# Kernel optimization log

Hardware: AMD Instinct MI355X
Metric: run time of the kernel (lower is better)

The kernel has to match this reference:

```python
import jax, jax.numpy as jnp
import numpy as np

B, T, IN, OUT, R = 4096, 8, 1024, 1024, 32

def setup_inputs() -> dict:
    key = jax.random.key(0)
    k1, k2, k3, k4 = jax.random.split(key, 4)
    return {
        "x": jax.random.normal(k1, (B, T, IN), dtype=jnp.float32),
        "first_shared_core": jax.random.normal(k2, (T, R), dtype=jnp.float32) * 0.1,
        "middle_shared_core": jax.random.normal(k3, (R, IN, R), dtype=jnp.float32) * 0.1,
        "task_core": jax.random.normal(k4, (R, OUT), dtype=jnp.float32) * 0.1,
    }

def reference(x, first_shared_core, middle_shared_core, task_core):
    # contract TT cores -> per-task weight [T, IN, OUT]
    w = jnp.einsum('tj,jik->tik', first_shared_core, middle_shared_core)
    w = jnp.einsum('tik,ko->tio', w, task_core)
    # per-task batched matmul: [B,T,IN] x [T,IN,OUT] -> [B,T,OUT]
    return jnp.einsum('bti,tio->bto', x, w)
```

## Files before the change

### kernel.cpp

```cpp
#include <hip/hip_runtime.h>
#include <hip/hip_bf16.h>
#include <stdint.h>

#define B_DIM 4096
#define T_DIM 8
#define IN_DIM 1024
#define OUT_DIM 1024
#define R_DIM 32

#define BM 256
#define BN 256
#define BK 64
#define NKT (IN_DIM / BK)

typedef __bf16 bf16x8 __attribute__((ext_vector_type(8)));
typedef float  f32x4  __attribute__((ext_vector_type(4)));

#define VMCNT(n) asm volatile("s_waitcnt vmcnt(" #n ")" ::: "memory")
#define CFENCE() asm volatile("" ::: "memory")
#define BARRIER() do { CFENCE(); __builtin_amdgcn_s_barrier(); CFENCE(); } while (0)


__device__ __forceinline__ uint32_t pack2_bf16(float a, float b) {
  uint32_t ua = __float_as_uint(a), ub = __float_as_uint(b);
  ua = (ua + 0x7FFFu + ((ua >> 16) & 1u)) >> 16;
  ub = (ub + 0x7FFFu + ((ub >> 16) & 1u)) & 0xFFFF0000u;
  return ua | ub;
}

__device__ __forceinline__ void gload_lds16(const void* g, void* l) {
  __builtin_amdgcn_global_load_lds(
      (const __attribute__((address_space(1))) void*)(uintptr_t)g,
      (__attribute__((address_space(3))) void*)(uint32_t)(uintptr_t)l,
      16, 0, 0);
}

__device__ __forceinline__ void stage_half(const uint16_t* gtile, int ktn,
                                           int half, uint8_t* ldsop,
                                           int wave, int lane) {
#pragma unroll
  for (int j = 0; j < 2; ++j) {
    int s = j * 64 + wave * 8 + (lane >> 3);
    int c = lane & 7;
    int row = (s >> 4) * 32 + half * 16 + (s & 15);
    gload_lds16((const uint8_t*)(gtile + (size_t)row * IN_DIM + ktn * BK) +
                    ((c ^ (s & 7)) << 4),
                ldsop + half * 16384 + j * 8192 + wave * 1024);
  }
}

__device__ __forceinline__ bf16x8 lds_frag(const uint8_t* op, int grp ,
                                           int par , int ks,
                                           int l15, int kg, int l7) {
  return *(const bf16x8*)(op + par * 16384 + (grp >> 1) * 2048 + l15 * 128 +
                          ((((ks << 2) + kg) ^ l7) << 4));
}

__global__ __launch_bounds__(256) void x_cvt(const float* __restrict__ x,
                                             uint16_t* __restrict__ xb) {
  int u = blockIdx.x * 256 + threadIdx.x;
  int i0 = (u & 127) << 3;
  int bt = u >> 7;
  int t = bt & 7, b = bt >> 3;
  const float4* src = (const float4*)(x + (size_t)bt * IN_DIM + i0);
  float4 v0 = src[0], v1 = src[1];
  uint4 o;
  o.x = pack2_bf16(v0.x, v0.y);
  o.y = pack2_bf16(v0.z, v0.w);
  o.z = pack2_bf16(v1.x, v1.y);
  o.w = pack2_bf16(v1.z, v1.w);
  *(uint4*)(xb + ((size_t)t * B_DIM + b) * IN_DIM + i0) = o;
}

__global__ void tt_stage1(const float* __restrict__ first,
                          const float* __restrict__ middle,
                          float* __restrict__ a1) {
  int idx = blockIdx.x * 256 + threadIdx.x;
  int t  = idx >> 15;
  int ik = idx & 32767;
  float acc = 0.f;
#pragma unroll
  for (int j = 0; j < R_DIM; ++j)
    acc = fmaf(first[t * R_DIM + j], middle[j * (IN_DIM * R_DIM) + ik], acc);
  a1[idx] = acc;
}

__global__ __launch_bounds__(256) void tt_stage2(const float* __restrict__ a1,
                                                 const float* __restrict__ task,
                                                 __hip_bfloat16* __restrict__ wT) {
  int bid = blockIdx.x;
  int t  = bid >> 8;
  int ob = (bid >> 4) & 15;
  int ib = bid & 15;
  __shared__ float A1s[64][33];
  __shared__ float Ts[32][64];
  int tid = threadIdx.x;
#pragma unroll
  for (int r = 0; r < 8; ++r) {
    int idx2 = tid + 256 * r;
    int il = idx2 >> 5, k = idx2 & 31;
    A1s[il][k] = a1[t * (IN_DIM * R_DIM) + (ib * 64 + il) * R_DIM + k];
  }
#pragma unroll
  for (int r = 0; r < 8; ++r) {
    int idx2 = tid + 256 * r;
    int k = idx2 >> 6, ol = idx2 & 63;
    Ts[k][ol] = task[k * OUT_DIM + ob * 64 + ol];
  }
  __syncthreads();
  int il = tid & 63;
  int og = tid >> 6;
  float acc[16];
#pragma unroll
  for (int r = 0; r < 16; ++r) acc[r] = 0.f;
#pragma unroll
  for (int k = 0; k < 32; ++k) {
    float a = A1s[il][k];
#pragma unroll
    for (int r = 0; r < 16; ++r)
      acc[r] = fmaf(a, Ts[k][og * 16 + r], acc[r]);
  }
#pragma unroll
  for (int r = 0; r < 16; ++r) {
    size_t o = (size_t)ob * 64 + og * 16 + r;
    wT[((size_t)t * OUT_DIM + o) * IN_DIM + ib * 64 + il] = __float2bfloat16(acc[r]);
  }
}

__global__ __launch_bounds__(512, 2) void tt_gemm(const uint16_t* __restrict__ XB,
                                                  const uint16_t* __restrict__ WT,
                                                  float* __restrict__ O) {
  extern __shared__ uint8_t sm[];
  int bid = blockIdx.x;
  const int t  = bid & 7;
  const int l  = bid >> 3;
  const int mt = l >> 2;
  const int nt = l & 3;

  const int tid  = threadIdx.x;
  const int lane = tid & 63;
  const int wave = tid >> 6;
  const int wr = wave >> 2, wc = wave & 3;
  const int wr8 = wr * 8, wc4 = wc * 4;
  const int l15 = lane & 15, l7 = lane & 7, kg = lane >> 4;

  const uint16_t* gA = XB + ((size_t)t * B_DIM + mt * BM) * IN_DIM;
  const uint16_t* gB = WT + ((size_t)t * OUT_DIM + nt * BN) * IN_DIM;

  f32x4 acc[8][4] = {};
  bf16x8 afr[4][2], bfr0[2][2], bfr1[2][2];

  stage_half(gA, 0, 0, sm, wave, lane);
  stage_half(gB, 0, 0, sm + 32768, wave, lane);
  stage_half(gA, 0, 1, sm, wave, lane);
  stage_half(gB, 0, 1, sm + 32768, wave, lane);
  VMCNT(0);
  BARRIER();

#pragma unroll 2
  for (int kt = 0; kt < NKT; ++kt) {
    const int P = kt & 1;
    const uint8_t* bA = sm + P * 65536;
    const uint8_t* bB = bA + 32768;
    uint8_t* nA = sm + (P ^ 1) * 65536;
    uint8_t* nB = nA + 32768;
    const bool st = (kt + 1) < NKT;

#pragma unroll
    for (int mo = 0; mo < 4; ++mo)
#pragma unroll
      for (int ks = 0; ks < 2; ++ks)
        afr[mo][ks] = lds_frag(bA, wr8 + mo * 2, 0, ks, l15, kg, l7);
#pragma unroll
    for (int no = 0; no < 2; ++no)
#pragma unroll
      for (int ks = 0; ks < 2; ++ks)
        bfr0[no][ks] = lds_frag(bB, wc4 + no * 2, 0, ks, l15, kg, l7);
    if (st) stage_half(gA, kt + 1, 0, nA, wave, lane);
    if (kt == NKT - 1) { VMCNT(0); } else { VMCNT(2); }
    BARRIER();
    __builtin_amdgcn_s_setprio(1);
#pragma unroll
    for (int mo = 0; mo < 4; ++mo)
#pragma unroll
      for (int no = 0; no < 2; ++no)
#pragma unroll
        for (int ks = 0; ks < 2; ++ks)
          acc[mo * 2][no * 2] = __builtin_amdgcn_mfma_f32_16x16x32_bf16(
              afr[mo][ks], bfr0[no][ks], acc[mo * 2][no * 2], 0, 0, 0);
    __builtin_amdgcn_s_setprio(0);
    BARRIER();

#pragma unroll
    for (int no = 0; no < 2; ++no)
#pragma unroll
      for (int ks = 0; ks < 2; ++ks)
        bfr1[no][ks] = lds_frag(bB, wc4 + no * 2 + 1, 1, ks, l15, kg, l7);
    if (st) stage_half(gB, kt + 1, 0, nB, wave, lane);
    BARRIER();
    __builtin_amdgcn_s_setprio(1);
#pragma unroll
    for (int mo = 0; mo < 4; ++mo)
#pragma unroll
      for (int no = 0; no < 2; ++no)
#pragma unroll
        for (int ks = 0; ks < 2; ++ks)
          acc[mo * 2][no * 2 + 1] = __builtin_amdgcn_mfma_f32_16x16x32_bf16(
              afr[mo][ks], bfr1[no][ks], acc[mo * 2][no * 2 + 1], 0, 0, 0);
    __builtin_amdgcn_s_setprio(0);
    BARRIER();

#pragma unroll
    for (int mo = 0; mo < 4; ++mo)
#pragma unroll
      for (int ks = 0; ks < 2; ++ks)
        afr[mo][ks] = lds_frag(bA, wr8 + mo * 2 + 1, 1, ks, l15, kg, l7);
    if (st) stage_half(gA, kt + 1, 1, nA, wave, lane);
    BARRIER();
    __builtin_amdgcn_s_setprio(1);
#pragma unroll
    for (int mo = 0; mo < 4; ++mo)
#pragma unroll
      for (int no = 0; no < 2; ++no)
#pragma unroll
        for (int ks = 0; ks < 2; ++ks)
          acc[mo * 2 + 1][no * 2] = __builtin_amdgcn_mfma_f32_16x16x32_bf16(
              afr[mo][ks], bfr0[no][ks], acc[mo * 2 + 1][no * 2], 0, 0, 0);
    __builtin_amdgcn_s_setprio(0);
    BARRIER();

    if (st) stage_half(gB, kt + 1, 1, nB, wave, lane);
    if (st) { VMCNT(4); }
    BARRIER();
    __builtin_amdgcn_s_setprio(1);
#pragma unroll
    for (int mo = 0; mo < 4; ++mo)
#pragma unroll
      for (int no = 0; no < 2; ++no)
#pragma unroll
        for (int ks = 0; ks < 2; ++ks)
          acc[mo * 2 + 1][no * 2 + 1] = __builtin_amdgcn_mfma_f32_16x16x32_bf16(
              afr[mo][ks], bfr1[no][ks], acc[mo * 2 + 1][no * 2 + 1], 0, 0, 0);
    __builtin_amdgcn_s_setprio(0);
    BARRIER();
  }

  const int crow0 = mt * BM + wr * 128 + (lane >> 4) * 4;
  const int ccol0 = nt * BN + wc * 64 + (lane & 15);
#pragma unroll
  for (int m = 0; m < 8; ++m) {
#pragma unroll
    for (int j = 0; j < 4; ++j) {
      size_t rowoff =
          ((size_t)(crow0 + m * 16 + j) * T_DIM + t) * OUT_DIM + ccol0;
#pragma unroll
      for (int n = 0; n < 4; ++n)
        O[rowoff + n * 16] = acc[m][n][j];
    }
  }
}

extern "C" void kernel_launch(void* const* d_in, const int* in_sizes, int n_in,
                              void* d_out, int out_size, void* d_ws, size_t ws_size,
                              hipStream_t stream) {
  const float* x      = (const float*)d_in[0];
  const float* first  = (const float*)d_in[1];
  const float* middle = (const float*)d_in[2];
  const float* task   = (const float*)d_in[3];
  float* out = (float*)d_out;

  float* a1 = (float*)d_ws;
  __hip_bfloat16* wT = (__hip_bfloat16*)((uint8_t*)d_ws + (1u << 20));
  uint16_t* xb = (uint16_t*)((uint8_t*)d_ws + (17u << 20));

  hipFuncSetAttribute((const void*)tt_gemm,
                      hipFuncAttributeMaxDynamicSharedMemorySize, 131072);

  x_cvt<<<(B_DIM * T_DIM * IN_DIM) / 8 / 256, 256, 0, stream>>>(x, xb);
  tt_stage1<<<(T_DIM * IN_DIM * R_DIM) / 256, 256, 0, stream>>>(first, middle, a1);
  tt_stage2<<<T_DIM * 16 * 16, 256, 0, stream>>>(a1, task, wT);
  tt_gemm<<<T_DIM * (B_DIM / BM) * (OUT_DIM / BN), 512, 131072, stream>>>(
      xb, (const uint16_t*)wT, out);
}
```

Before: 138.0 us.

## Fuse fp32-to-bf16 conversion of x into GEMM A-tile staging

Removes the separate x_cvt kernel and its bf16 workspace copy. The GEMM now loads fp32 x rows straight into registers, converts them to bf16 and writes them swizzled into LDS. Global-to-LDS direct loads are kept for the weight tile only, and the last k-iteration is peeled out of the loop. This avoids one full extra read and write pass over x (about 128MB fp32 in, 64MB bf16 out), but each GEMM tile now reads twice the A bytes. It also adds register pressure and VALU conversion work inside the main loop.

```diff
diff --git a/kernel.cpp b/kernel.cpp
--- a/kernel.cpp
+++ b/kernel.cpp
@@ -17,6 +17,7 @@
 typedef float  f32x4  __attribute__((ext_vector_type(4)));
 
 #define VMCNT(n) asm volatile("s_waitcnt vmcnt(" #n ")" ::: "memory")
+#define LGKM0()  asm volatile("s_waitcnt lgkmcnt(0)" ::: "memory")
 #define CFENCE() asm volatile("" ::: "memory")
 #define BARRIER() do { CFENCE(); __builtin_amdgcn_s_barrier(); CFENCE(); } while (0)
 
@@ -49,27 +50,35 @@
   }
 }
 
-__device__ __forceinline__ bf16x8 lds_frag(const uint8_t* op, int grp ,
-                                           int par , int ks,
+__device__ __forceinline__ bf16x8 lds_frag(const uint8_t* op, int grp,
+                                           int par, int ks,
                                            int l15, int kg, int l7) {
   return *(const bf16x8*)(op + par * 16384 + (grp >> 1) * 2048 + l15 * 128 +
                           ((((ks << 2) + kg) ^ l7) << 4));
 }
 
-__global__ __launch_bounds__(256) void x_cvt(const float* __restrict__ x,
-                                             uint16_t* __restrict__ xb) {
-  int u = blockIdx.x * 256 + threadIdx.x;
-  int i0 = (u & 127) << 3;
-  int bt = u >> 7;
-  int t = bt & 7, b = bt >> 3;
-  const float4* src = (const float4*)(x + (size_t)bt * IN_DIM + i0);
-  float4 v0 = src[0], v1 = src[1];
-  uint4 o;
-  o.x = pack2_bf16(v0.x, v0.y);
-  o.y = pack2_bf16(v0.z, v0.w);
-  o.z = pack2_bf16(v1.x, v1.y);
-  o.w = pack2_bf16(v1.z, v1.w);
-  *(uint4*)(xb + ((size_t)t * B_DIM + b) * IN_DIM + i0) = o;
+__device__ __forceinline__ void a_issue(const float* gax, int kt, int qp,
+                                        float4 ar[2][2]) {
+#pragma unroll
+  for (int qq = 0; qq < 2; ++qq)
+#pragma unroll
+    for (int h = 0; h < 2; ++h)
+      ar[qq][h] = *(const float4*)(gax +
+          (size_t)(qp * 2 + qq) * 8 * (T_DIM * IN_DIM) + kt * BK + h * 4);
+}
+
+__device__ __forceinline__ void a_cvt_write(uint8_t* nA, int awbase, int qp,
+                                            float4 ar[2][2]) {
+#pragma unroll
+  for (int qq = 0; qq < 2; ++qq) {
+    int q = qp * 2 + qq;
+    uint4 o;
+    o.x = pack2_bf16(ar[qq][0].x, ar[qq][0].y);
+    o.y = pack2_bf16(ar[qq][0].z, ar[qq][0].w);
+    o.z = pack2_bf16(ar[qq][1].x, ar[qq][1].y);
+    o.w = pack2_bf16(ar[qq][1].z, ar[qq][1].w);
+    *(uint4*)(nA + ((q >> 1) & 1) * 16384 + (q & 1) * 1024 + awbase) = o;
+  }
 }
 
 __global__ void tt_stage1(const float* __restrict__ first,
@@ -127,7 +136,7 @@
   }
 }
 
-__global__ __launch_bounds__(512, 2) void tt_gemm(const uint16_t* __restrict__ XB,
+__global__ __launch_bounds__(512, 2) void tt_gemm(const float* __restrict__ X,
                                                   const uint16_t* __restrict__ WT,
                                                   float* __restrict__ O) {
   extern __shared__ uint8_t sm[];
@@ -144,27 +153,37 @@
   const int wr8 = wr * 8, wc4 = wc * 4;
   const int l15 = lane & 15, l7 = lane & 7, kg = lane >> 4;
 
-  const uint16_t* gA = XB + ((size_t)t * B_DIM + mt * BM) * IN_DIM;
+  const int arow_in = lane >> 3;
+  const float* gax = X +
+      ((size_t)(mt * BM + wave * 32 + arow_in) * T_DIM + t) * IN_DIM +
+      (lane & 7) * 8;
+  const int awbase = wave * 2048 + arow_in * 128 + (((lane & 7) ^ arow_in) << 4);
+
   const uint16_t* gB = WT + ((size_t)t * OUT_DIM + nt * BN) * IN_DIM;
 
   f32x4 acc[8][4] = {};
   bf16x8 afr[4][2], bfr0[2][2], bfr1[2][2];
-
-  stage_half(gA, 0, 0, sm, wave, lane);
+  float4 ar[2][2];
+
+  a_issue(gax, 0, 0, ar);
+  VMCNT(0);
+  a_cvt_write(sm, awbase, 0, ar);
+  a_issue(gax, 0, 1, ar);
+  VMCNT(0);
+  a_cvt_write(sm, awbase, 1, ar);
   stage_half(gB, 0, 0, sm + 32768, wave, lane);
-  stage_half(gA, 0, 1, sm, wave, lane);
   stage_half(gB, 0, 1, sm + 32768, wave, lane);
   VMCNT(0);
+  LGKM0();
   BARRIER();
 
 #pragma unroll 2
-  for (int kt = 0; kt < NKT; ++kt) {
+  for (int kt = 0; kt < NKT - 1; ++kt) {
     const int P = kt & 1;
     const uint8_t* bA = sm + P * 65536;
     const uint8_t* bB = bA + 32768;
     uint8_t* nA = sm + (P ^ 1) * 65536;
     uint8_t* nB = nA + 32768;
-    const bool st = (kt + 1) < NKT;
 
 #pragma unroll
     for (int mo = 0; mo < 4; ++mo)
@@ -176,8 +195,8 @@
 #pragma unroll
       for (int ks = 0; ks < 2; ++ks)
         bfr0[no][ks] = lds_frag(bB, wc4 + no * 2, 0, ks, l15, kg, l7);
-    if (st) stage_half(gA, kt + 1, 0, nA, wave, lane);
-    if (kt == NKT - 1) { VMCNT(0); } else { VMCNT(2); }
+    stage_half(gB, kt + 1, 0, nB, wave, lane);
+    a_issue(gax, kt + 1, 0, ar);
     BARRIER();
     __builtin_amdgcn_s_setprio(1);
 #pragma unroll
@@ -196,7 +215,7 @@
 #pragma unroll
       for (int ks = 0; ks < 2; ++ks)
         bfr1[no][ks] = lds_frag(bB, wc4 + no * 2 + 1, 1, ks, l15, kg, l7);
-    if (st) stage_half(gB, kt + 1, 0, nB, wave, lane);
+    stage_half(gB, kt + 1, 1, nB, wave, lane);
     BARRIER();
     __builtin_amdgcn_s_setprio(1);
 #pragma unroll
@@ -215,7 +234,14 @@
 #pragma unroll
       for (int ks = 0; ks < 2; ++ks)
         afr[mo][ks] = lds_frag(bA, wr8 + mo * 2 + 1, 1, ks, l15, kg, l7);
-    if (st) stage_half(gA, kt + 1, 1, nA, wave, lane);
+#pragma unroll
+    for (int no = 0; no < 2; ++no)
+#pragma unroll
+      for (int ks = 0; ks < 2; ++ks)
+        bfr0[no][ks] = lds_frag(bB, wc4 + no * 2, 0, ks, l15, kg, l7);
+    VMCNT(2);
+    a_cvt_write(nA, awbase, 0, ar);
+    a_issue(gax, kt + 1, 1, ar);
     BARRIER();
     __builtin_amdgcn_s_setprio(1);
 #pragma unroll
@@ -229,8 +255,9 @@
     __builtin_amdgcn_s_setprio(0);
     BARRIER();
 
-    if (st) stage_half(gB, kt + 1, 1, nB, wave, lane);
-    if (st) { VMCNT(4); }
+    VMCNT(0);
+    a_cvt_write(nA, awbase, 1, ar);
+    LGKM0();
     BARRIER();
     __builtin_amdgcn_s_setprio(1);
 #pragma unroll
@@ -243,6 +270,58 @@
               afr[mo][ks], bfr1[no][ks], acc[mo * 2 + 1][no * 2 + 1], 0, 0, 0);
     __builtin_amdgcn_s_setprio(0);
     BARRIER();
+  }
+
+  {
+    const uint8_t* bA = sm + 65536;
+    const uint8_t* bB = bA + 32768;
+#pragma unroll
+    for (int mo = 0; mo < 4; ++mo)
+#pragma unroll
+      for (int ks = 0; ks < 2; ++ks)
+        afr[mo][ks] = lds_frag(bA, wr8 + mo * 2, 0, ks, l15, kg, l7);
+#pragma unroll
+    for (int no = 0; no < 2; ++no)
+#pragma unroll
+      for (int ks = 0; ks < 2; ++ks)
+        bfr0[no][ks] = lds_frag(bB, wc4 + no * 2, 0, ks, l15, kg, l7);
+#pragma unroll
+    for (int no = 0; no < 2; ++no)
+#pragma unroll
+      for (int ks = 0; ks < 2; ++ks)
+        bfr1[no][ks] = lds_frag(bB, wc4 + no * 2 + 1, 1, ks, l15, kg, l7);
+#pragma unroll
+    for (int mo = 0; mo < 4; ++mo)
+#pragma unroll
+      for (int no = 0; no < 2; ++no)
+#pragma unroll
+        for (int ks = 0; ks < 2; ++ks)
+          acc[mo * 2][no * 2] = __builtin_amdgcn_mfma_f32_16x16x32_bf16(
+              afr[mo][ks], bfr0[no][ks], acc[mo * 2][no * 2], 0, 0, 0);
+#pragma unroll
+    for (int mo = 0; mo < 4; ++mo)
+#pragma unroll
+      for (int no = 0; no < 2; ++no)
+#pragma unroll
+        for (int ks = 0; ks < 2; ++ks)
+          acc[mo * 2][no * 2 + 1] = __builtin_amdgcn_mfma_f32_16x16x32_bf16(
+              afr[mo][ks], bfr1[no][ks], acc[mo * 2][no * 2 + 1], 0, 0, 0);
+#pragma unroll
+    for (int mo = 0; mo < 4; ++mo)
+#pragma unroll
+      for (int ks = 0; ks < 2; ++ks)
+        afr[mo][ks] = lds_frag(bA, wr8 + mo * 2 + 1, 1, ks, l15, kg, l7);
+#pragma unroll
+    for (int mo = 0; mo < 4; ++mo)
+#pragma unroll
+      for (int no = 0; no < 2; ++no)
+#pragma unroll
+        for (int ks = 0; ks < 2; ++ks) {
+          acc[mo * 2 + 1][no * 2] = __builtin_amdgcn_mfma_f32_16x16x32_bf16(
+              afr[mo][ks], bfr0[no][ks], acc[mo * 2 + 1][no * 2], 0, 0, 0);
+          acc[mo * 2 + 1][no * 2 + 1] = __builtin_amdgcn_mfma_f32_16x16x32_bf16(
+              afr[mo][ks], bfr1[no][ks], acc[mo * 2 + 1][no * 2 + 1], 0, 0, 0);
+        }
   }
 
   const int crow0 = mt * BM + wr * 128 + (lane >> 4) * 4;
@@ -271,14 +350,12 @@
 
   float* a1 = (float*)d_ws;
   __hip_bfloat16* wT = (__hip_bfloat16*)((uint8_t*)d_ws + (1u << 20));
-  uint16_t* xb = (uint16_t*)((uint8_t*)d_ws + (17u << 20));
 
   hipFuncSetAttribute((const void*)tt_gemm,
                       hipFuncAttributeMaxDynamicSharedMemorySize, 131072);
 
-  x_cvt<<<(B_DIM * T_DIM * IN_DIM) / 8 / 256, 256, 0, stream>>>(x, xb);
   tt_stage1<<<(T_DIM * IN_DIM * R_DIM) / 256, 256, 0, stream>>>(first, middle, a1);
   tt_stage2<<<T_DIM * 16 * 16, 256, 0, stream>>>(a1, task, wT);
   tt_gemm<<<T_DIM * (B_DIM / BM) * (OUT_DIM / BN), 512, 131072, stream>>>(
-      xb, (const uint16_t*)wT, out);
-}
+      x, (const uint16_t*)wT, out);
+}
```

New measurement: 156.3 us. 13.3% more time.

## Overlap x conversion with weight contraction and split GEMM by task halves

Applied to the files above, without the earlier changes.

Fuses the fp32-to-bf16 conversion of x into the TT-core contraction kernels and the first GEMM launch. Tasks 0-3 are converted alongside stage1, tasks 4-5 alongside stage2, and tasks 6-7 at the tail of a first GEMM over tasks 0-3, followed by a second GEMM over tasks 4-7. This hides part of the memory-bound conversion behind the compute-light stages and cuts one launch. The cost is two smaller GEMM launches of 256 blocks each, which may underfill the GPU, plus extra tail work in the first GEMM.

```diff
diff --git a/kernel.cpp b/kernel.cpp
--- a/kernel.cpp
+++ b/kernel.cpp
@@ -49,91 +49,118 @@
   }
 }
 
-__device__ __forceinline__ bf16x8 lds_frag(const uint8_t* op, int grp ,
-                                           int par , int ks,
+__device__ __forceinline__ bf16x8 lds_frag(const uint8_t* op, int grp,
+                                           int par, int ks,
                                            int l15, int kg, int l7) {
   return *(const bf16x8*)(op + par * 16384 + (grp >> 1) * 2048 + l15 * 128 +
                           ((((ks << 2) + kg) ^ l7) << 4));
 }
 
-__global__ __launch_bounds__(256) void x_cvt(const float* __restrict__ x,
-                                             uint16_t* __restrict__ xb) {
-  int u = blockIdx.x * 256 + threadIdx.x;
-  int i0 = (u & 127) << 3;
-  int bt = u >> 7;
-  int t = bt & 7, b = bt >> 3;
-  const float4* src = (const float4*)(x + (size_t)bt * IN_DIM + i0);
-  float4 v0 = src[0], v1 = src[1];
-  uint4 o;
-  o.x = pack2_bf16(v0.x, v0.y);
-  o.y = pack2_bf16(v0.z, v0.w);
-  o.z = pack2_bf16(v1.x, v1.y);
-  o.w = pack2_bf16(v1.z, v1.w);
-  *(uint4*)(xb + ((size_t)t * B_DIM + b) * IN_DIM + i0) = o;
-}
-
-__global__ void tt_stage1(const float* __restrict__ first,
-                          const float* __restrict__ middle,
-                          float* __restrict__ a1) {
-  int idx = blockIdx.x * 256 + threadIdx.x;
-  int t  = idx >> 15;
-  int ik = idx & 32767;
-  float acc = 0.f;
-#pragma unroll
-  for (int j = 0; j < R_DIM; ++j)
-    acc = fmaf(first[t * R_DIM + j], middle[j * (IN_DIM * R_DIM) + ik], acc);
-  a1[idx] = acc;
-}
-
-__global__ __launch_bounds__(256) void tt_stage2(const float* __restrict__ a1,
-                                                 const float* __restrict__ task,
-                                                 __hip_bfloat16* __restrict__ wT) {
+__device__ __forceinline__ void cvt32(const float* src, uint16_t* dst) {
+  float4 v[8];
+#pragma unroll
+  for (int i = 0; i < 8; ++i) v[i] = *(const float4*)(src + i * 4);
+#pragma unroll
+  for (int i = 0; i < 4; ++i) {
+    uint4 o;
+    o.x = pack2_bf16(v[2 * i].x, v[2 * i].y);
+    o.y = pack2_bf16(v[2 * i].z, v[2 * i].w);
+    o.z = pack2_bf16(v[2 * i + 1].x, v[2 * i + 1].y);
+    o.w = pack2_bf16(v[2 * i + 1].z, v[2 * i + 1].w);
+    *(uint4*)(dst + i * 8) = o;
+  }
+}
+
+__global__ __launch_bounds__(256) void pre1(const float* __restrict__ first,
+                                            const float* __restrict__ middle,
+                                            float* __restrict__ a1,
+                                            const float* __restrict__ x,
+                                            uint16_t* __restrict__ xb) {
+  int bid = blockIdx.x, tid = threadIdx.x;
+  if (bid < 1024) {
+    int idx = bid * 256 + tid;
+    int t  = idx >> 15;
+    int ik = idx & 32767;
+    float acc = 0.f;
+#pragma unroll
+    for (int j = 0; j < R_DIM; ++j)
+      acc = fmaf(first[t * R_DIM + j], middle[j * (IN_DIM * R_DIM) + ik], acc);
+    a1[idx] = acc;
+  } else {
+    int cb = bid - 1024;
+    int row_in = tid >> 5;
+    int c0 = (tid & 31) * 32;
+    int R = cb * 8 + row_in;
+    int b = R >> 2, t = R & 3;
+    cvt32(x + ((size_t)b * T_DIM + t) * IN_DIM + c0,
+          xb + ((size_t)t * B_DIM + b) * IN_DIM + c0);
+  }
+}
+
+__global__ __launch_bounds__(256) void pre2(const float* __restrict__ a1,
+                                            const float* __restrict__ task,
+                                            __hip_bfloat16* __restrict__ wT,
+                                            const float* __restrict__ x,
+                                            uint16_t* __restrict__ xb) {
   int bid = blockIdx.x;
-  int t  = bid >> 8;
-  int ob = (bid >> 4) & 15;
-  int ib = bid & 15;
-  __shared__ float A1s[64][33];
-  __shared__ float Ts[32][64];
   int tid = threadIdx.x;
-#pragma unroll
-  for (int r = 0; r < 8; ++r) {
-    int idx2 = tid + 256 * r;
-    int il = idx2 >> 5, k = idx2 & 31;
-    A1s[il][k] = a1[t * (IN_DIM * R_DIM) + (ib * 64 + il) * R_DIM + k];
-  }
-#pragma unroll
-  for (int r = 0; r < 8; ++r) {
-    int idx2 = tid + 256 * r;
-    int k = idx2 >> 6, ol = idx2 & 63;
-    Ts[k][ol] = task[k * OUT_DIM + ob * 64 + ol];
-  }
-  __syncthreads();
-  int il = tid & 63;
-  int og = tid >> 6;
-  float acc[16];
-#pragma unroll
-  for (int r = 0; r < 16; ++r) acc[r] = 0.f;
-#pragma unroll
-  for (int k = 0; k < 32; ++k) {
-    float a = A1s[il][k];
-#pragma unroll
-    for (int r = 0; r < 16; ++r)
-      acc[r] = fmaf(a, Ts[k][og * 16 + r], acc[r]);
-  }
-#pragma unroll
-  for (int r = 0; r < 16; ++r) {
-    size_t o = (size_t)ob * 64 + og * 16 + r;
-    wT[((size_t)t * OUT_DIM + o) * IN_DIM + ib * 64 + il] = __float2bfloat16(acc[r]);
+  if (bid < 2048) {
+    int t  = bid >> 8;
+    int ob = (bid >> 4) & 15;
+    int ib = bid & 15;
+    __shared__ float A1s[64][33];
+    __shared__ float Ts[32][64];
+#pragma unroll
+    for (int r = 0; r < 8; ++r) {
+      int idx2 = tid + 256 * r;
+      int il = idx2 >> 5, k = idx2 & 31;
+      A1s[il][k] = a1[t * (IN_DIM * R_DIM) + (ib * 64 + il) * R_DIM + k];
+    }
+#pragma unroll
+    for (int r = 0; r < 8; ++r) {
+      int idx2 = tid + 256 * r;
+      int k = idx2 >> 6, ol = idx2 & 63;
+      Ts[k][ol] = task[k * OUT_DIM + ob * 64 + ol];
+    }
+    __syncthreads();
+    int il = tid & 63;
+    int og = tid >> 6;
+    float acc[16];
+#pragma unroll
+    for (int r = 0; r < 16; ++r) acc[r] = 0.f;
+#pragma unroll
+    for (int k = 0; k < 32; ++k) {
+      float a = A1s[il][k];
+#pragma unroll
+      for (int r = 0; r < 16; ++r)
+        acc[r] = fmaf(a, Ts[k][og * 16 + r], acc[r]);
+    }
+#pragma unroll
+    for (int r = 0; r < 16; ++r) {
+      size_t o = (size_t)ob * 64 + og * 16 + r;
+      wT[((size_t)t * OUT_DIM + o) * IN_DIM + ib * 64 + il] = __float2bfloat16(acc[r]);
+    }
+  } else {
+    int cb = bid - 2048;
+    int row_in = tid >> 5;
+    int c0 = (tid & 31) * 32;
+    int R = cb * 8 + row_in;
+    int b = R >> 1, t = 4 + (R & 1);
+    cvt32(x + ((size_t)b * T_DIM + t) * IN_DIM + c0,
+          xb + ((size_t)t * B_DIM + b) * IN_DIM + c0);
   }
 }
 
 __global__ __launch_bounds__(512, 2) void tt_gemm(const uint16_t* __restrict__ XB,
                                                   const uint16_t* __restrict__ WT,
-                                                  float* __restrict__ O) {
+                                                  float* __restrict__ O,
+                                                  const float* __restrict__ Xf,
+                                                  uint16_t* __restrict__ XBw,
+                                                  int t_base, int doCvt) {
   extern __shared__ uint8_t sm[];
   int bid = blockIdx.x;
-  const int t  = bid & 7;
-  const int l  = bid >> 3;
+  const int t  = t_base + (bid & 3);
+  const int l  = bid >> 2;
   const int mt = l >> 2;
   const int nt = l & 3;
 
@@ -258,6 +285,17 @@
         O[rowoff + n * 16] = acc[m][n][j];
     }
   }
+
+  if (doCvt) {
+    const int row_in = tid >> 4;
+    const int c0 = (tid & 15) * 64;
+    const int R = bid * 32 + row_in;
+    const int b = R >> 1, tt2 = 6 + (R & 1);
+    const float* src = Xf + ((size_t)b * T_DIM + tt2) * IN_DIM + c0;
+    uint16_t* dst = XBw + ((size_t)tt2 * B_DIM + b) * IN_DIM + c0;
+    cvt32(src, dst);
+    cvt32(src + 32, dst + 32);
+  }
 }
 
 extern "C" void kernel_launch(void* const* d_in, const int* in_sizes, int n_in,
@@ -276,9 +314,10 @@
   hipFuncSetAttribute((const void*)tt_gemm,
                       hipFuncAttributeMaxDynamicSharedMemorySize, 131072);
 
-  x_cvt<<<(B_DIM * T_DIM * IN_DIM) / 8 / 256, 256, 0, stream>>>(x, xb);
-  tt_stage1<<<(T_DIM * IN_DIM * R_DIM) / 256, 256, 0, stream>>>(first, middle, a1);
-  tt_stage2<<<T_DIM * 16 * 16, 256, 0, stream>>>(a1, task, wT);
-  tt_gemm<<<T_DIM * (B_DIM / BM) * (OUT_DIM / BN), 512, 131072, stream>>>(
-      xb, (const uint16_t*)wT, out);
-}
+  pre1<<<3072, 256, 0, stream>>>(first, middle, a1, x, xb);
+  pre2<<<3072, 256, 0, stream>>>(a1, task, wT, x, xb);
+  tt_gemm<<<256, 512, 131072, stream>>>(xb, (const uint16_t*)wT, out,
+                                        x, xb, 0, 1);
+  tt_gemm<<<256, 512, 131072, stream>>>(xb, (const uint16_t*)wT, out,
+                                        x, xb, 4, 0);
+}
```

Measured after the change: 160.9 us. 16.6% more time.

## Fuse fp32-to-bf16 conversion of x into GEMM LDS fragment loads

Applied to the files above, without the earlier changes.

Drops the separate x_cvt kernel, so the bf16 copy of x is no longer written to and read back from memory. The GEMM now stages fp32 x tiles straight into LDS and converts them to bf16 in registers with byte-permute truncation while building the A fragments. To fit the larger fp32 A tile, LDS drops from a double buffer to a single buffer with reworked staging points and waits, which can expose load latency. Truncation also replaces round-to-nearest-even, which slightly lowers accuracy.

```diff
diff --git a/kernel.cpp b/kernel.cpp
--- a/kernel.cpp
+++ b/kernel.cpp
@@ -21,13 +21,6 @@
 #define BARRIER() do { CFENCE(); __builtin_amdgcn_s_barrier(); CFENCE(); } while (0)
 
 
-__device__ __forceinline__ uint32_t pack2_bf16(float a, float b) {
-  uint32_t ua = __float_as_uint(a), ub = __float_as_uint(b);
-  ua = (ua + 0x7FFFu + ((ua >> 16) & 1u)) >> 16;
-  ub = (ub + 0x7FFFu + ((ub >> 16) & 1u)) & 0xFFFF0000u;
-  return ua | ub;
-}
-
 __device__ __forceinline__ void gload_lds16(const void* g, void* l) {
   __builtin_amdgcn_global_load_lds(
       (const __attribute__((address_space(1))) void*)(uintptr_t)g,
@@ -35,9 +28,9 @@
       16, 0, 0);
 }
 
-__device__ __forceinline__ void stage_half(const uint16_t* gtile, int ktn,
-                                           int half, uint8_t* ldsop,
-                                           int wave, int lane) {
+__device__ __forceinline__ void stage_half_b(const uint16_t* gtile, int ktn,
+                                             int half, uint8_t* ldsop,
+                                             int wave, int lane) {
 #pragma unroll
   for (int j = 0; j < 2; ++j) {
     int s = j * 64 + wave * 8 + (lane >> 3);
@@ -49,27 +42,38 @@
   }
 }
 
-__device__ __forceinline__ bf16x8 lds_frag(const uint8_t* op, int grp ,
-                                           int par , int ks,
-                                           int l15, int kg, int l7) {
-  return *(const bf16x8*)(op + par * 16384 + (grp >> 1) * 2048 + l15 * 128 +
+__device__ __forceinline__ void stage_half_a(const float* xpanel, int ktn,
+                                             int half, uint8_t* ldsA,
+                                             int wave, int lane) {
+#pragma unroll
+  for (int j = 0; j < 4; ++j) {
+    int s = j * 32 + wave * 4 + (lane >> 4);
+    int c = lane & 15;
+    int row = (s >> 4) * 32 + half * 16 + (s & 15);
+    gload_lds16(xpanel + (size_t)row * (T_DIM * IN_DIM) + ktn * BK +
+                    ((c ^ (s & 7)) << 2),
+                ldsA + half * 32768 + j * 8192 + wave * 1024);
+  }
+}
+
+__device__ __forceinline__ bf16x8 b_frag(const uint8_t* opB, int grp, int par,
+                                         int ks, int l15, int kg, int l7) {
+  return *(const bf16x8*)(opB + par * 16384 + (grp >> 1) * 2048 + l15 * 128 +
                           ((((ks << 2) + kg) ^ l7) << 4));
 }
 
-__global__ __launch_bounds__(256) void x_cvt(const float* __restrict__ x,
-                                             uint16_t* __restrict__ xb) {
-  int u = blockIdx.x * 256 + threadIdx.x;
-  int i0 = (u & 127) << 3;
-  int bt = u >> 7;
-  int t = bt & 7, b = bt >> 3;
-  const float4* src = (const float4*)(x + (size_t)bt * IN_DIM + i0);
-  float4 v0 = src[0], v1 = src[1];
-  uint4 o;
-  o.x = pack2_bf16(v0.x, v0.y);
-  o.y = pack2_bf16(v0.z, v0.w);
-  o.z = pack2_bf16(v1.x, v1.y);
-  o.w = pack2_bf16(v1.z, v1.w);
-  *(uint4*)(xb + ((size_t)t * B_DIM + b) * IN_DIM + i0) = o;
+__device__ __forceinline__ bf16x8 a_frag(const uint8_t* opA, int grp2, int half,
+                                         int ks, int l15, int kg, int l7) {
+  const uint8_t* base = opA + half * 32768 + grp2 * 4096 + l15 * 256;
+  const int c0 = ks * 8 + kg * 2;
+  f32x4 lo = *(const f32x4*)(base + (((c0    ) ^ l7) << 4));
+  f32x4 hi = *(const f32x4*)(base + (((c0 + 1) ^ l7) << 4));
+  union { uint32_t u[4]; bf16x8 v; } cv;
+  cv.u[0] = __builtin_amdgcn_perm(__float_as_uint(lo.y), __float_as_uint(lo.x), 0x07060302u);
+  cv.u[1] = __builtin_amdgcn_perm(__float_as_uint(lo.w), __float_as_uint(lo.z), 0x07060302u);
+  cv.u[2] = __builtin_amdgcn_perm(__float_as_uint(hi.y), __float_as_uint(hi.x), 0x07060302u);
+  cv.u[3] = __builtin_amdgcn_perm(__float_as_uint(hi.w), __float_as_uint(hi.z), 0x07060302u);
+  return cv.v;
 }
 
 __global__ void tt_stage1(const float* __restrict__ first,
@@ -127,7 +131,7 @@
   }
 }
 
-__global__ __launch_bounds__(512, 2) void tt_gemm(const uint16_t* __restrict__ XB,
+__global__ __launch_bounds__(512, 2) void tt_gemm(const float* __restrict__ X,
                                                   const uint16_t* __restrict__ WT,
                                                   float* __restrict__ O) {
   extern __shared__ uint8_t sm[];
@@ -141,43 +145,39 @@
   const int lane = tid & 63;
   const int wave = tid >> 6;
   const int wr = wave >> 2, wc = wave & 3;
-  const int wr8 = wr * 8, wc4 = wc * 4;
+  const int wc4 = wc * 4;
   const int l15 = lane & 15, l7 = lane & 7, kg = lane >> 4;
 
-  const uint16_t* gA = XB + ((size_t)t * B_DIM + mt * BM) * IN_DIM;
+  const float* xpanel = X + ((size_t)(mt * BM) * T_DIM + t) * IN_DIM;
   const uint16_t* gB = WT + ((size_t)t * OUT_DIM + nt * BN) * IN_DIM;
+
+  uint8_t* bA = sm;
+  uint8_t* bB = sm + 65536;
 
   f32x4 acc[8][4] = {};
   bf16x8 afr[4][2], bfr0[2][2], bfr1[2][2];
 
-  stage_half(gA, 0, 0, sm, wave, lane);
-  stage_half(gB, 0, 0, sm + 32768, wave, lane);
-  stage_half(gA, 0, 1, sm, wave, lane);
-  stage_half(gB, 0, 1, sm + 32768, wave, lane);
-  VMCNT(0);
+  stage_half_a(xpanel, 0, 0, bA, wave, lane);
+  stage_half_b(gB, 0, 0, bB, wave, lane);
+  stage_half_a(xpanel, 0, 1, bA, wave, lane);
+  stage_half_b(gB, 0, 1, bB, wave, lane);
+  VMCNT(6);
   BARRIER();
 
-#pragma unroll 2
   for (int kt = 0; kt < NKT; ++kt) {
-    const int P = kt & 1;
-    const uint8_t* bA = sm + P * 65536;
-    const uint8_t* bB = bA + 32768;
-    uint8_t* nA = sm + (P ^ 1) * 65536;
-    uint8_t* nB = nA + 32768;
     const bool st = (kt + 1) < NKT;
 
 #pragma unroll
     for (int mo = 0; mo < 4; ++mo)
 #pragma unroll
       for (int ks = 0; ks < 2; ++ks)
-        afr[mo][ks] = lds_frag(bA, wr8 + mo * 2, 0, ks, l15, kg, l7);
+        afr[mo][ks] = a_frag(bA, wr * 4 + mo, 0, ks, l15, kg, l7);
 #pragma unroll
     for (int no = 0; no < 2; ++no)
 #pragma unroll
       for (int ks = 0; ks < 2; ++ks)
-        bfr0[no][ks] = lds_frag(bB, wc4 + no * 2, 0, ks, l15, kg, l7);
-    if (st) stage_half(gA, kt + 1, 0, nA, wave, lane);
-    if (kt == NKT - 1) { VMCNT(0); } else { VMCNT(2); }
+        bfr0[no][ks] = b_frag(bB, wc4 + no * 2, 0, ks, l15, kg, l7);
+    VMCNT(0);
     BARRIER();
     __builtin_amdgcn_s_setprio(1);
 #pragma unroll
@@ -195,8 +195,11 @@
     for (int no = 0; no < 2; ++no)
 #pragma unroll
       for (int ks = 0; ks < 2; ++ks)
-        bfr1[no][ks] = lds_frag(bB, wc4 + no * 2 + 1, 1, ks, l15, kg, l7);
-    if (st) stage_half(gB, kt + 1, 0, nB, wave, lane);
+        bfr1[no][ks] = b_frag(bB, wc4 + no * 2 + 1, 1, ks, l15, kg, l7);
+    if (st) {
+      stage_half_a(xpanel, kt + 1, 0, bA, wave, lane);
+      stage_half_b(gB, kt + 1, 0, bB, wave, lane);
+    }
     BARRIER();
     __builtin_amdgcn_s_setprio(1);
 #pragma unroll
@@ -214,8 +217,7 @@
     for (int mo = 0; mo < 4; ++mo)
 #pragma unroll
       for (int ks = 0; ks < 2; ++ks)
-        afr[mo][ks] = lds_frag(bA, wr8 + mo * 2 + 1, 1, ks, l15, kg, l7);
-    if (st) stage_half(gA, kt + 1, 1, nA, wave, lane);
+        afr[mo][ks] = a_frag(bA, wr * 4 + mo, 1, ks, l15, kg, l7);
     BARRIER();
     __builtin_amdgcn_s_setprio(1);
 #pragma unroll
@@ -229,8 +231,11 @@
     __builtin_amdgcn_s_setprio(0);
     BARRIER();
 
-    if (st) stage_half(gB, kt + 1, 1, nB, wave, lane);
-    if (st) { VMCNT(4); }
+    if (st) {
+      stage_half_a(xpanel, kt + 1, 1, bA, wave, lane);
+      stage_half_b(gB, kt + 1, 1, bB, wave, lane);
+    }
+    VMCNT(6);
     BARRIER();
     __builtin_amdgcn_s_setprio(1);
 #pragma unroll
@@ -271,14 +276,12 @@
 
   float* a1 = (float*)d_ws;
   __hip_bfloat16* wT = (__hip_bfloat16*)((uint8_t*)d_ws + (1u << 20));
-  uint16_t* xb = (uint16_t*)((uint8_t*)d_ws + (17u << 20));
 
   hipFuncSetAttribute((const void*)tt_gemm,
-                      hipFuncAttributeMaxDynamicSharedMemorySize, 131072);
-
-  x_cvt<<<(B_DIM * T_DIM * IN_DIM) / 8 / 256, 256, 0, stream>>>(x, xb);
+                      hipFuncAttributeMaxDynamicSharedMemorySize, 98304);
+
   tt_stage1<<<(T_DIM * IN_DIM * R_DIM) / 256, 256, 0, stream>>>(first, middle, a1);
   tt_stage2<<<T_DIM * 16 * 16, 256, 0, stream>>>(a1, task, wT);
-  tt_gemm<<<T_DIM * (B_DIM / BM) * (OUT_DIM / BN), 512, 131072, stream>>>(
-      xb, (const uint16_t*)wT, out);
-}
+  tt_gemm<<<T_DIM * (B_DIM / BM) * (OUT_DIM / BN), 512, 98304, stream>>>(
+      x, (const uint16_t*)wT, out);
+}
```

New measurement: 136.3 us. Within noise of the previous version (-1.3%).
